# Optimization experiments

Hardware: AMD Instinct MI355X
Metric: run time of the kernel (lower is better)

## Reference

```python
import jax, jax.numpy as jnp
import numpy as np

N, E, G = 100000, 500000, 1000


def _gat(h_in, src, dst, W, a_s, a_d, b, n):
    # PyG GATConv, heads=1, concat=True, negative_slope=0.2, self-loops already in src/dst
    h = h_in @ W.T                                  # [N, out]
    alpha_src = h @ a_s                             # [N]
    alpha_dst = h @ a_d                             # [N]
    e = jax.nn.leaky_relu(alpha_src[src] + alpha_dst[dst], 0.2)  # [E']
    m = jax.ops.segment_max(e, dst, num_segments=n)
    ex = jnp.exp(e - m[dst])
    den = jax.ops.segment_sum(ex, dst, num_segments=n)
    alpha = ex / den[dst]                           # segment softmax over incoming edges
    out = jax.ops.segment_sum(h[src] * alpha[:, None], dst, num_segments=n)
    return out + b


def _forward(x, edge_index, batch, w1, b1, w2, b2, w3, b3,
             g1w, g1as, g1ad, g1b, g2w, g2as, g2ad, g2b,
             g3w, g3as, g3ad, g3b, g4w, g4as, g4ad, g4b,
             g5w, g5as, g5ad, g5b, lw, lb):
    n = x.shape[0]
    h = jax.nn.relu(x @ w1.T + b1)
    h = jax.nn.relu(h @ w2.T + b2)
    h = jax.nn.relu(h @ w3.T + b3)
    loops = jnp.arange(n)
    src = jnp.concatenate([edge_index[0], loops])   # add self-loops
    dst = jnp.concatenate([edge_index[1], loops])
    h = jax.nn.relu(_gat(h, src, dst, g1w, g1as, g1ad, g1b, n))
    h = jax.nn.relu(_gat(h, src, dst, g2w, g2as, g2ad, g2b, n))
    h = jax.nn.relu(_gat(h, src, dst, g3w, g3as, g3ad, g3b, n))
    h = jax.nn.relu(_gat(h, src, dst, g4w, g4as, g4ad, g4b, n))
    h = jax.nn.relu(_gat(h, src, dst, g5w, g5as, g5ad, g5b, n))
    sums = jax.ops.segment_sum(h, batch, num_segments=G)            # [G,32]
    cnt = jax.ops.segment_sum(jnp.ones((n,), h.dtype), batch, num_segments=G)
    mean = sums / jnp.maximum(cnt, 1.0)[:, None]
    return jax.nn.sigmoid(mean @ lw.T + lb)         # [G,1]


def setup_inputs() -> dict:
    key = jax.random.key(0)
    ks = jax.random.split(key, 24)

    def lin(k, o, i):
        k1, k2 = jax.random.split(k)
        s = 1.0 / np.sqrt(i)
        return (jax.random.uniform(k1, (o, i), jnp.float32, -s, s),
                jax.random.uniform(k2, (o,), jnp.float32, -s, s))

    def gat_p(k, i, o):
        k1, k2, k3 = jax.random.split(k, 3)
        s = 1.0 / np.sqrt(i)
        W = jax.random.uniform(k1, (o, i), jnp.float32, -s, s)
        a_s = jax.random.normal(k2, (o,), jnp.float32) / np.sqrt(o)
        a_d = jax.random.normal(k3, (o,), jnp.float32) / np.sqrt(o)
        return W, a_s, a_d, jnp.zeros((o,), jnp.float32)

    inp = {}
    inp['x'] = jax.random.normal(ks[0], (N, 1), jnp.float32)
    inp['edge_index'] = jax.random.randint(ks[1], (2, E), 0, N)
    inp['batch'] = jnp.sort(jax.random.randint(ks[2], (N,), 0, G))
    inp['w1'], inp['b1'] = lin(ks[3], 16, 1)
    inp['w2'], inp['b2'] = lin(ks[4], 32, 16)
    inp['w3'], inp['b3'] = lin(ks[5], 64, 32)
    dims = [(64, 128), (128, 256), (256, 128), (128, 64), (64, 32)]
    for j, (i, o) in enumerate(dims, start=1):
        W, a_s, a_d, b = gat_p(ks[5 + j], i, o)
        inp[f'g{j}w'], inp[f'g{j}as'], inp[f'g{j}ad'], inp[f'g{j}b'] = W, a_s, a_d, b
    inp['lw'], inp['lb'] = lin(ks[12], 1, 32)
    return inp


def reference(x, edge_index, batch, w1, b1, w2, b2, w3, b3,
              g1w, g1as, g1ad, g1b, g2w, g2as, g2ad, g2b,
              g3w, g3as, g3ad, g3b, g4w, g4as, g4ad, g4b,
              g5w, g5as, g5ad, g5b, lw, lb):
    return _forward(x, edge_index, batch, w1, b1, w2, b2, w3, b3,
                    g1w, g1as, g1ad, g1b, g2w, g2as, g2ad, g2b,
                    g3w, g3as, g3ad, g3b, g4w, g4as, g4ad, g4b,
                    g5w, g5as, g5ad, g5b, lw, lb)
```

## Files before the change

### kernel.cpp

```cpp
#include <hip/hip_runtime.h>
#include <math.h>

typedef __attribute__((ext_vector_type(8))) __bf16 bf16x8;
typedef __attribute__((ext_vector_type(4))) float f32x4;

__device__ inline unsigned short f2bf(float f) {
    unsigned int i = __float_as_uint(f);
    unsigned int r = i + 0x7fffu + ((i >> 16) & 1u);
    return (unsigned short)(r >> 16);
}
__device__ inline float bf2f(unsigned short u) {
    return __uint_as_float(((unsigned int)u) << 16);
}

__global__ __launch_bounds__(256) void prelude_kernel(
    const float* __restrict__ x,
    const float* __restrict__ w1, const float* __restrict__ b1,
    const float* __restrict__ w2, const float* __restrict__ b2,
    const float* __restrict__ w3, const float* __restrict__ b3,
    unsigned short* __restrict__ h0, int n,
    const float* __restrict__ g0, const float* __restrict__ g1, const float* __restrict__ g2,
    const float* __restrict__ g3, const float* __restrict__ g4,
    unsigned short* __restrict__ wbAll,
    const int* __restrict__ batch, int* __restrict__ gstart, int G,
    const int* __restrict__ dst, int* __restrict__ deg, int E,
    int mlpB, int f2bfB, int gsB, int histB,
    const float* __restrict__ as1, const float* __restrict__ ad1,
    float* __restrict__ s1out, float* __restrict__ d1out,
    const float* __restrict__ as2, const float* __restrict__ ad2,
    float* __restrict__ pv2) {
    int b = blockIdx.x;
    int tid = threadIdx.x;
    if (b < mlpB) {
        __shared__ float sw1[16], sb1[16], sw2[32 * 16], sb2[32], sw3[64 * 32], sb3[64];
        __shared__ float ps1[64], pd1[64];
        if (tid < 16) { sw1[tid] = w1[tid]; sb1[tid] = b1[tid]; }
        if (tid < 32) sb2[tid] = b2[tid];
        if (tid < 64) sb3[tid] = b3[tid];
        for (int i = tid; i < 512; i += 256) sw2[i] = w2[i];
        for (int i = tid; i < 2048; i += 256) sw3[i] = w3[i];
        if (tid >= 192) {
            int i = tid - 192;
            float s = 0.f, d = 0.f;
            for (int o = 0; o < 128; o++) {
                float w = g0[o * 64 + i];
                s += as1[o] * w;
                d += ad1[o] * w;
            }
            ps1[i] = s;
            pd1[i] = d;
        }
        __syncthreads();
        int node = b * 256 + tid;
        if (node >= n) return;
        float xv = x[node];
        float t1[16], t2[32];
#pragma unroll
        for (int i = 0; i < 16; i++) t1[i] = fmaxf(sw1[i] * xv + sb1[i], 0.f);
#pragma unroll
        for (int o = 0; o < 32; o++) {
            float a = sb2[o];
#pragma unroll
            for (int i = 0; i < 16; i++) a += sw2[o * 16 + i] * t1[i];
            t2[o] = fmaxf(a, 0.f);
        }
        float sdot = 0.f, ddot = 0.f;
        uint4* gp = (uint4*)(h0 + (size_t)node * 64);
#pragma unroll
        for (int c = 0; c < 8; c++) {
            unsigned int wvec[4];
#pragma unroll
            for (int p = 0; p < 4; p++) {
                int o = c * 8 + p * 2;
                float a0 = sb3[o], a1 = sb3[o + 1];
#pragma unroll
                for (int i = 0; i < 32; i++) {
                    a0 += sw3[o * 32 + i] * t2[i];
                    a1 += sw3[(o + 1) * 32 + i] * t2[i];
                }
                float r0 = fmaxf(a0, 0.f), r1 = fmaxf(a1, 0.f);
                sdot += r0 * ps1[o] + r1 * ps1[o + 1];
                ddot += r0 * pd1[o] + r1 * pd1[o + 1];
                wvec[p] = (unsigned)f2bf(r0) | ((unsigned)f2bf(r1) << 16);
            }
            gp[c] = make_uint4(wvec[0], wvec[1], wvec[2], wvec[3]);
        }
        s1out[node] = sdot;
        d1out[node] = ddot;
    } else if (b < mlpB + f2bfB) {
        int i = (b - mlpB) * 256 + tid;
        float v;
        if (i < 8192) v = g0[i];
        else if (i < 40960) v = g1[i - 8192];
        else if (i < 73728) v = g2[i - 40960];
        else if (i < 81920) v = g3[i - 73728];
        else if (i < 83968) v = g4[i - 81920];
        else return;
        wbAll[i] = f2bf(v);
    } else if (b < mlpB + f2bfB + gsB) {
        int g = (b - mlpB - f2bfB) * 256 + tid;
        if (g > G) return;
        if (g == G) { gstart[G] = n; return; }
        int lo = 0, hi = n;
        while (lo < hi) {
            int mid = (lo + hi) >> 1;
            if (batch[mid] < g) lo = mid + 1;
            else hi = mid;
        }
        gstart[g] = lo;
    } else if (b < mlpB + f2bfB + gsB + histB) {
        int e = (b - mlpB - f2bfB - gsB) * 256 + tid;
        if (e >= E + n) return;
        int d = (e < E) ? dst[e] : (e - E);
        atomicAdd(&deg[d], 1);
    } else {
        if (tid < 128) {
            float s = 0.f;
            for (int o = 0; o < 256; o++) s += as2[o] * g1[o * 128 + tid];
            pv2[tid] = s;
        } else {
            int c = tid - 128;
            float s = 0.f;
            for (int o = 0; o < 256; o++) s += ad2[o] * g1[o * 128 + c];
            pv2[128 + c] = s;
        }
    }
}

template <int BN, int EPI>
__global__ __launch_bounds__(256) void gemm_mfma(
    const unsigned short* __restrict__ A, const unsigned short* __restrict__ Wb,
    unsigned short* __restrict__ Cb,
    const float* __restrict__ avs, const float* __restrict__ avd,
    float* __restrict__ as_, float* __restrict__ ad_,
    const float* __restrict__ bias, int n, int K, int O) {
    constexpr int SN = BN / 32;
    __shared__ unsigned short As[128][72];
    __shared__ unsigned short Ws[BN][72];
    int tid = threadIdx.x;
    int row0 = blockIdx.x * 128, col0 = blockIdx.y * BN;
    int w = tid >> 6, lane = tid & 63;
    int wr = w >> 1, wc = w & 1;
    int quad = lane >> 4, l15 = lane & 15;
    f32x4 acc[4][SN];
#pragma unroll
    for (int mi = 0; mi < 4; mi++)
#pragma unroll
        for (int ni = 0; ni < SN; ni++) acc[mi][ni] = (f32x4){0.f, 0.f, 0.f, 0.f};

    for (int k0 = 0; k0 < K; k0 += 64) {
#pragma unroll
        for (int i = tid; i < 1024; i += 256) {
            int r = i >> 3, c8 = i & 7;
            int gr = row0 + r;
            uint4 v = make_uint4(0u, 0u, 0u, 0u);
            if (gr < n) v = *(const uint4*)(A + (size_t)gr * K + k0 + c8 * 8);
            *(uint4*)&As[r][c8 * 8] = v;
        }
#pragma unroll
        for (int i = tid; i < BN * 8; i += 256) {
            int r = i >> 3, c8 = i & 7;
            uint4 v = *(const uint4*)(Wb + (size_t)(col0 + r) * K + k0 + c8 * 8);
            *(uint4*)&Ws[r][c8 * 8] = v;
        }
        __syncthreads();
#pragma unroll
        for (int kk = 0; kk < 64; kk += 32) {
            bf16x8 bfr[SN];
#pragma unroll
            for (int ni = 0; ni < SN; ni++)
                bfr[ni] = *(const bf16x8*)&Ws[wc * (BN / 2) + ni * 16 + l15][kk + quad * 8];
#pragma unroll
            for (int mi = 0; mi < 4; mi++) {
                bf16x8 afr = *(const bf16x8*)&As[wr * 64 + mi * 16 + l15][kk + quad * 8];
#pragma unroll
                for (int ni = 0; ni < SN; ni++)
                    acc[mi][ni] = __builtin_amdgcn_mfma_f32_16x16x32_bf16(afr, bfr[ni],
                                                                          acc[mi][ni], 0, 0, 0);
            }
        }
        __syncthreads();
    }
    float avsv[SN], avdv[SN], bv[SN];
    int gc[SN];
#pragma unroll
    for (int ni = 0; ni < SN; ni++) {
        gc[ni] = col0 + wc * (BN / 2) + ni * 16 + l15;
        if constexpr (EPI != 2) {
            avsv[ni] = avs[gc[ni]];
            avdv[ni] = avd[gc[ni]];
        }
        if constexpr (EPI >= 1) bv[ni] = bias[gc[ni]];
    }
#pragma unroll
    for (int mi = 0; mi < 4; mi++) {
        int gm0 = row0 + wr * 64 + mi * 16 + quad * 4;
        float ps[4] = {0.f, 0.f, 0.f, 0.f}, pd[4] = {0.f, 0.f, 0.f, 0.f};
#pragma unroll
        for (int ni = 0; ni < SN; ni++) {
#pragma unroll
            for (int r = 0; r < 4; r++) {
                float d = acc[mi][ni][r];
                if constexpr (EPI >= 1) d = fmaxf(d + bv[ni], 0.f);
                int gm = gm0 + r;
                if (gm < n) Cb[(size_t)gm * O + gc[ni]] = f2bf(d);
                if constexpr (EPI != 2) {
                    ps[r] += d * avsv[ni];
                    pd[r] += d * avdv[ni];
                }
            }
        }
        if constexpr (EPI != 2) {
#pragma unroll
            for (int r = 0; r < 4; r++) {
#pragma unroll
                for (int m = 1; m <= 8; m <<= 1) {
                    ps[r] += __shfl_xor(ps[r], m);
                    pd[r] += __shfl_xor(pd[r], m);
                }
            }
            if (l15 == 0) {
#pragma unroll
                for (int r = 0; r < 4; r++) {
                    int gm = gm0 + r;
                    if (gm < n) {
                        atomicAdd(&as_[gm], ps[r]);
                        atomicAdd(&ad_[gm], pd[r]);
                    }
                }
            }
        }
    }
}

__global__ void scan_block_sums(const int* __restrict__ deg, int* __restrict__ bsums, int n) {
    __shared__ int sdata[256];
    int tid = threadIdx.x;
    int base = blockIdx.x * 1024 + tid * 4;
    int s = 0;
    for (int i = 0; i < 4; i++) {
        int g = base + i;
        if (g < n) s += deg[g];
    }
    sdata[tid] = s;
    __syncthreads();
    for (int off = 128; off > 0; off >>= 1) {
        if (tid < off) sdata[tid] += sdata[tid + off];
        __syncthreads();
    }
    if (tid == 0) bsums[blockIdx.x] = sdata[0];
}

__global__ void scan_write(const int* __restrict__ deg, const int* __restrict__ bsums,
                           int* __restrict__ rowptr, int* __restrict__ cursor, int n, int nb) {
    __shared__ int sdata[256];
    int tid = threadIdx.x;
    sdata[tid] = (tid < blockIdx.x && tid < nb) ? bsums[tid] : 0;
    __syncthreads();
    for (int off = 128; off > 0; off >>= 1) {
        if (tid < off) sdata[tid] += sdata[tid + off];
        __syncthreads();
    }
    int base = sdata[0];
    __syncthreads();
    int gbase = blockIdx.x * 1024 + tid * 4;
    int v[4];
    int s = 0;
    for (int i = 0; i < 4; i++) {
        int g = gbase + i;
        v[i] = (g < n) ? deg[g] : 0;
        s += v[i];
    }
    sdata[tid] = s;
    __syncthreads();
    for (int off = 1; off < 256; off <<= 1) {
        int t = (tid >= off) ? sdata[tid - off] : 0;
        __syncthreads();
        sdata[tid] += t;
        __syncthreads();
    }
    int excl = sdata[tid] - s + base;
    for (int i = 0; i < 4; i++) {
        int g = gbase + i;
        if (g < n) { rowptr[g] = excl; cursor[g] = excl; }
        excl += v[i];
    }
    if (blockIdx.x == gridDim.x - 1 && tid == 255) rowptr[n] = base + sdata[255];
}

__global__ void scatter_kernel(const int* __restrict__ esrc_in, const int* __restrict__ edst_in,
                               int* __restrict__ cursor, int* __restrict__ esrc, int E, int n) {
    int e = blockIdx.x * 256 + threadIdx.x;
    if (e >= E + n) return;
    int s, d;
    if (e < E) { s = esrc_in[e]; d = edst_in[e]; }
    else { s = e - E; d = e - E; }
    int pos = atomicAdd(&cursor[d], 1);
    esrc[pos] = s;
}

template <int O, bool BIASRELU>
__global__ __launch_bounds__(256) void gat_aggregate(
    const unsigned short* __restrict__ hl, const float* __restrict__ as_,
    const float* __restrict__ ad_, const int* __restrict__ rowptr,
    const int* __restrict__ esrc, const float* __restrict__ bias,
    unsigned short* __restrict__ hout, int n, float* __restrict__ zeroBuf, int zeroCnt) {
    int gtid = blockIdx.x * 256 + threadIdx.x;
    if (gtid < zeroCnt) zeroBuf[gtid] = 0.f;
    constexpr int C8 = O / 8;
    constexpr int EPP = 16 / C8;
    int tid = threadIdx.x;
    int v = blockIdx.x * 16 + (tid >> 4);
    int l = tid & 15;
    int gbase = tid & 48;
    if (v >= n) return;
    int beg = rowptr[v], end = rowptr[v + 1];
    int deg = end - beg;
    float adv = ad_[v];
    int sub = l / C8;
    int c = l % C8;
    float acc[8] = {0.f, 0.f, 0.f, 0.f, 0.f, 0.f, 0.f, 0.f};
    if (deg <= 16) {
        int sreg = v;
        float e = -1e30f;
        if (l < deg) {
            sreg = esrc[beg + l];
            float t = as_[sreg] + adv;
            e = (t > 0.f) ? t : 0.2f * t;
        }
        float m = e;
#pragma unroll
        for (int o = 8; o > 0; o >>= 1) m = fmaxf(m, __shfl_xor(m, o));
        float ex = (l < deg) ? __expf(e - m) : 0.f;
        float sum = ex;
#pragma unroll
        for (int o = 8; o > 0; o >>= 1) sum += __shfl_xor(sum, o);
        float alpha_r = ex / sum;
        for (int j0 = 0; j0 < deg; j0 += EPP) {
            int idx = j0 + sub;
            int cidx = (idx < deg) ? idx : 0;
            float alpha = __shfl(alpha_r, gbase + cidx);
            int s2 = __shfl(sreg, gbase + cidx);
            if (idx >= deg) alpha = 0.f;
            uint4 raw = ((const uint4*)(hl + (size_t)s2 * O))[c];
            acc[0] += alpha * __uint_as_float(raw.x << 16);
            acc[1] += alpha * __uint_as_float(raw.x & 0xffff0000u);
            acc[2] += alpha * __uint_as_float(raw.y << 16);
            acc[3] += alpha * __uint_as_float(raw.y & 0xffff0000u);
            acc[4] += alpha * __uint_as_float(raw.z << 16);
            acc[5] += alpha * __uint_as_float(raw.z & 0xffff0000u);
            acc[6] += alpha * __uint_as_float(raw.w << 16);
            acc[7] += alpha * __uint_as_float(raw.w & 0xffff0000u);
        }
    } else {
        float mymax = -1e30f;
        for (int j = beg + l; j < end; j += 16) {
            float e = as_[esrc[j]] + adv;
            e = (e > 0.f) ? e : 0.2f * e;
            mymax = fmaxf(mymax, e);
        }
#pragma unroll
        for (int o = 8; o > 0; o >>= 1) mymax = fmaxf(mymax, __shfl_xor(mymax, o));
        float mysum = 0.f;
        for (int j = beg + l; j < end; j += 16) {
            float e = as_[esrc[j]] + adv;
            e = (e > 0.f) ? e : 0.2f * e;
            mysum += __expf(e - mymax);
        }
#pragma unroll
        for (int o = 8; o > 0; o >>= 1) mysum += __shfl_xor(mysum, o);
        float invden = 1.f / mysum;
        for (int j0 = beg; j0 < end; j0 += EPP) {
            int j = j0 + sub;
            bool valid = j < end;
            int s = valid ? esrc[j] : v;
            float e = as_[s] + adv;
            e = (e > 0.f) ? e : 0.2f * e;
            float alpha = valid ? __expf(e - mymax) * invden : 0.f;
            uint4 raw = ((const uint4*)(hl + (size_t)s * O))[c];
            acc[0] += alpha * __uint_as_float(raw.x << 16);
            acc[1] += alpha * __uint_as_float(raw.x & 0xffff0000u);
            acc[2] += alpha * __uint_as_float(raw.y << 16);
            acc[3] += alpha * __uint_as_float(raw.y & 0xffff0000u);
            acc[4] += alpha * __uint_as_float(raw.z << 16);
            acc[5] += alpha * __uint_as_float(raw.z & 0xffff0000u);
            acc[6] += alpha * __uint_as_float(raw.w << 16);
            acc[7] += alpha * __uint_as_float(raw.w & 0xffff0000u);
        }
    }
#pragma unroll
    for (int o = C8; o < 16; o <<= 1)
#pragma unroll
        for (int k = 0; k < 8; k++) acc[k] += __shfl_xor(acc[k], o);
    if (l < C8) {
        unsigned short ov[8];
#pragma unroll
        for (int k = 0; k < 8; k++) {
            float val = acc[k];
            if constexpr (BIASRELU) val = fmaxf(val + bias[c * 8 + k], 0.f);
            ov[k] = f2bf(val);
        }
        uint4 packed;
        packed.x = (unsigned)ov[0] | ((unsigned)ov[1] << 16);
        packed.y = (unsigned)ov[2] | ((unsigned)ov[3] << 16);
        packed.z = (unsigned)ov[4] | ((unsigned)ov[5] << 16);
        packed.w = (unsigned)ov[6] | ((unsigned)ov[7] << 16);
        ((uint4*)(hout + (size_t)v * O))[c] = packed;
    }
}

__global__ __launch_bounds__(256) void pool_final_kernel(
    const unsigned short* __restrict__ h, const int* __restrict__ start,
    const float* __restrict__ lw, const float* __restrict__ lb,
    float* __restrict__ out, int G) {
    __shared__ float red[8][33];
    int g = blockIdx.x;
    if (g >= G) return;
    int beg = start[g], end = start[g + 1];
    int tid = threadIdx.x;
    int nodeLane = tid >> 5, f = tid & 31;
    float acc = 0.f;
    for (int v = beg + nodeLane; v < end; v += 8)
        acc += bf2f(h[(size_t)v * 32 + f]);
    red[nodeLane][f] = acc;
    __syncthreads();
    if (tid < 32) {
        float s = 0.f;
#pragma unroll
        for (int i = 0; i < 8; i++) s += red[i][f];
        float inv = 1.f / fmaxf((float)(end - beg), 1.f);
        float val = s * inv * lw[f];
#pragma unroll
        for (int o = 16; o > 0; o >>= 1) val += __shfl_xor(val, o);
        if (f == 0) out[g] = 1.f / (1.f + __expf(-(val + lb[0])));
    }
}

extern "C" void kernel_launch(void* const* d_in, const int* in_sizes, int n_in,
                              void* d_out, int out_size, void* d_ws, size_t ws_size,
                              hipStream_t stream) {
    const float* x = (const float*)d_in[0];
    const int* ei = (const int*)d_in[1];
    const int* batch = (const int*)d_in[2];
    const float* w1 = (const float*)d_in[3];
    const float* b1 = (const float*)d_in[4];
    const float* w2 = (const float*)d_in[5];
    const float* b2 = (const float*)d_in[6];
    const float* w3 = (const float*)d_in[7];
    const float* b3 = (const float*)d_in[8];
    const float* gw[5];
    const float* gas[5];
    const float* gad[5];
    const float* gb[5];
    for (int l = 0; l < 5; l++) {
        gw[l] = (const float*)d_in[9 + l * 4 + 0];
        gas[l] = (const float*)d_in[9 + l * 4 + 1];
        gad[l] = (const float*)d_in[9 + l * 4 + 2];
        gb[l] = (const float*)d_in[9 + l * 4 + 3];
    }
    const float* lw = (const float*)d_in[29];
    const float* lb = (const float*)d_in[30];
    float* out = (float*)d_out;

    int N = in_sizes[0];
    int E = in_sizes[1] / 2;
    int G = out_size;
    int Etot = E + N;

    char* ws = (char*)d_ws;
    size_t off = 0;
    auto alloc = [&](size_t bytes) -> void* {
        void* p = ws + off;
        off = (off + bytes + 255) & ~(size_t)255;
        return p;
    };
    unsigned short* actA = (unsigned short*)alloc((size_t)N * 256 * 2);
    unsigned short* actB = (unsigned short*)alloc((size_t)N * 256 * 2);
    char* zblock = (char*)alloc((size_t)N * 20);
    float* sd2 = (float*)zblock;
    float* sd3 = sd2 + (size_t)N * 2;
    int* deg = (int*)(zblock + (size_t)N * 16);
    float* sd1 = (float*)alloc((size_t)N * 2 * 4);
    float* pv2 = (float*)alloc(256 * 4);
    int* rowptr = (int*)alloc((size_t)(N + 1) * 4);
    int* cursor = (int*)alloc((size_t)(N + 1) * 4);
    int* esrc = (int*)alloc((size_t)Etot * 4);
    int* bsums = (int*)alloc(4096);
    int* gstart = (int*)alloc((size_t)(G + 1) * 4);
    unsigned short* wbAll = (unsigned short*)alloc((size_t)83968 * 2);
    const int woff[5] = {0, 8192, 40960, 73728, 81920};
    unsigned short* wb[5];
    for (int l = 0; l < 5; l++) wb[l] = wbAll + woff[l];
    (void)ws_size;
    (void)n_in;

    hipMemsetAsync(zblock, 0, (size_t)N * 20, stream);

    int mlpB = (N + 255) / 256;
    int f2bfB = (83968 + 255) / 256;
    int gsB = (G + 1 + 255) / 256;
    int histB = (Etot + 255) / 256;
    prelude_kernel<<<mlpB + f2bfB + gsB + histB + 1, 256, 0, stream>>>(
        x, w1, b1, w2, b2, w3, b3, actA, N, gw[0], gw[1], gw[2], gw[3], gw[4], wbAll, batch,
        gstart, G, ei + E, deg, E, mlpB, f2bfB, gsB, histB,
        gas[0], gad[0], sd1, sd1 + N, gas[1], gad[1], pv2);

    int nb = (N + 1023) / 1024;
    scan_block_sums<<<nb, 256, 0, stream>>>(deg, bsums, N);
    scan_write<<<nb, 256, 0, stream>>>(deg, bsums, rowptr, cursor, N, nb);
    scatter_kernel<<<(Etot + 255) / 256, 256, 0, stream>>>(ei, ei + E, cursor, esrc, E, N);

    int aggBlocks = (N + 15) / 16;
    int gx = (N + 127) / 128;

    gat_aggregate<64, false><<<aggBlocks, 256, 0, stream>>>(
        actA, sd1, sd1 + N, rowptr, esrc, nullptr, actB, N, nullptr, 0);
    {
        dim3 grid(gx, 2);
        gemm_mfma<64, 1><<<grid, 256, 0, stream>>>(actB, wb[0], actA, pv2, pv2 + 128, sd2,
                                                   sd2 + N, gb[0], N, 64, 128);
    }

    gat_aggregate<128, false><<<aggBlocks, 256, 0, stream>>>(
        actA, sd2, sd2 + N, rowptr, esrc, nullptr, actB, N, sd1, 2 * N);
    {
        dim3 grid(gx, 4);
        gemm_mfma<64, 2><<<grid, 256, 0, stream>>>(actB, wb[1], actA, nullptr, nullptr,
                                                   nullptr, nullptr, gb[1], N, 128, 256);
    }

    {
        dim3 grid(gx, 2);
        gemm_mfma<64, 0><<<grid, 256, 0, stream>>>(actA, wb[2], actB, gas[2], gad[2], sd3,
                                                   sd3 + N, nullptr, N, 256, 128);
    }
    gat_aggregate<128, true><<<aggBlocks, 256, 0, stream>>>(
        actB, sd3, sd3 + N, rowptr, esrc, gb[2], actA, N, sd2, 2 * N);

    {
        dim3 grid(gx, 1);
        gemm_mfma<64, 0><<<grid, 256, 0, stream>>>(actA, wb[3], actB, gas[3], gad[3], sd1,
                                                   sd1 + N, nullptr, N, 128, 64);
    }
    gat_aggregate<64, true><<<aggBlocks, 256, 0, stream>>>(
        actB, sd1, sd1 + N, rowptr, esrc, gb[3], actA, N, nullptr, 0);

    {
        dim3 grid(gx, 1);
        gemm_mfma<32, 0><<<grid, 256, 0, stream>>>(actA, wb[4], actB, gas[4], gad[4], sd2,
                                                   sd2 + N, nullptr, N, 64, 32);
    }
    gat_aggregate<32, true><<<aggBlocks, 256, 0, stream>>>(
        actB, sd2, sd2 + N, rowptr, esrc, gb[4], actA, N, nullptr, 0);

    pool_final_kernel<<<G, 256, 0, stream>>>(actA, gstart, lw, lb, out, G);
}
```

Baseline: 462.1 us.

## Read MLP weights directly from global memory and widen GEMM column tiles to 128

The prelude MLP no longer stages its weights in shared memory. It reads w1/w2/w3 straight from global memory as float4 vectors, which are uniform across threads and likely go to scalar or cached loads. The attention projection vectors are packed into one float4 shared array. Three GEMM launches now use 128-wide column tiles with half as many column blocks, so each block reuses its A tile across more outputs, at the cost of more registers per block and fewer blocks.

```diff
diff --git a/kernel.cpp b/kernel.cpp
--- a/kernel.cpp
+++ b/kernel.cpp
@@ -32,13 +32,7 @@
     int b = blockIdx.x;
     int tid = threadIdx.x;
     if (b < mlpB) {
-        __shared__ float sw1[16], sb1[16], sw2[32 * 16], sb2[32], sw3[64 * 32], sb3[64];
-        __shared__ float ps1[64], pd1[64];
-        if (tid < 16) { sw1[tid] = w1[tid]; sb1[tid] = b1[tid]; }
-        if (tid < 32) sb2[tid] = b2[tid];
-        if (tid < 64) sb3[tid] = b3[tid];
-        for (int i = tid; i < 512; i += 256) sw2[i] = w2[i];
-        for (int i = tid; i < 2048; i += 256) sw3[i] = w3[i];
+        __shared__ float4 psd1q[32];
         if (tid >= 192) {
             int i = tid - 192;
             float s = 0.f, d = 0.f;
@@ -47,8 +41,7 @@
                 s += as1[o] * w;
                 d += ad1[o] * w;
             }
-            ps1[i] = s;
-            pd1[i] = d;
+            ((float2*)psd1q)[i] = make_float2(s, d);
         }
         __syncthreads();
         int node = b * 256 + tid;
@@ -56,14 +49,20 @@
         float xv = x[node];
         float t1[16], t2[32];
 #pragma unroll
-        for (int i = 0; i < 16; i++) t1[i] = fmaxf(sw1[i] * xv + sb1[i], 0.f);
+        for (int i = 0; i < 16; i++) t1[i] = fmaxf(w1[i] * xv + b1[i], 0.f);
+        const float4* w2v = (const float4*)w2;
 #pragma unroll
         for (int o = 0; o < 32; o++) {
-            float a = sb2[o];
-#pragma unroll
-            for (int i = 0; i < 16; i++) a += sw2[o * 16 + i] * t1[i];
+            float a = b2[o];
+#pragma unroll
+            for (int q = 0; q < 4; q++) {
+                float4 wv = w2v[o * 4 + q];
+                a += wv.x * t1[q * 4] + wv.y * t1[q * 4 + 1] + wv.z * t1[q * 4 + 2] +
+                     wv.w * t1[q * 4 + 3];
+            }
             t2[o] = fmaxf(a, 0.f);
         }
+        const float4* w3v = (const float4*)w3;
         float sdot = 0.f, ddot = 0.f;
         uint4* gp = (uint4*)(h0 + (size_t)node * 64);
 #pragma unroll
@@ -72,15 +71,20 @@
 #pragma unroll
             for (int p = 0; p < 4; p++) {
                 int o = c * 8 + p * 2;
-                float a0 = sb3[o], a1 = sb3[o + 1];
-#pragma unroll
-                for (int i = 0; i < 32; i++) {
-                    a0 += sw3[o * 32 + i] * t2[i];
-                    a1 += sw3[(o + 1) * 32 + i] * t2[i];
+                float a0 = b3[o], a1 = b3[o + 1];
+#pragma unroll
+                for (int q = 0; q < 8; q++) {
+                    float4 wa = w3v[o * 8 + q];
+                    float4 wb = w3v[o * 8 + 8 + q];
+                    a0 += wa.x * t2[q * 4] + wa.y * t2[q * 4 + 1] + wa.z * t2[q * 4 + 2] +
+                          wa.w * t2[q * 4 + 3];
+                    a1 += wb.x * t2[q * 4] + wb.y * t2[q * 4 + 1] + wb.z * t2[q * 4 + 2] +
+                          wb.w * t2[q * 4 + 3];
                 }
                 float r0 = fmaxf(a0, 0.f), r1 = fmaxf(a1, 0.f);
-                sdot += r0 * ps1[o] + r1 * ps1[o + 1];
-                ddot += r0 * pd1[o] + r1 * pd1[o + 1];
+                float4 qsd = psd1q[o >> 1];
+                sdot += r0 * qsd.x + r1 * qsd.z;
+                ddot += r0 * qsd.y + r1 * qsd.w;
                 wvec[p] = (unsigned)f2bf(r0) | ((unsigned)f2bf(r1) << 16);
             }
             gp[c] = make_uint4(wvec[0], wvec[1], wvec[2], wvec[3]);
@@ -516,23 +520,23 @@
     gat_aggregate<64, false><<<aggBlocks, 256, 0, stream>>>(
         actA, sd1, sd1 + N, rowptr, esrc, nullptr, actB, N, nullptr, 0);
     {
-        dim3 grid(gx, 2);
-        gemm_mfma<64, 1><<<grid, 256, 0, stream>>>(actB, wb[0], actA, pv2, pv2 + 128, sd2,
-                                                   sd2 + N, gb[0], N, 64, 128);
+        dim3 grid(gx, 1);
+        gemm_mfma<128, 1><<<grid, 256, 0, stream>>>(actB, wb[0], actA, pv2, pv2 + 128, sd2,
+                                                    sd2 + N, gb[0], N, 64, 128);
     }
 
     gat_aggregate<128, false><<<aggBlocks, 256, 0, stream>>>(
         actA, sd2, sd2 + N, rowptr, esrc, nullptr, actB, N, sd1, 2 * N);
     {
-        dim3 grid(gx, 4);
-        gemm_mfma<64, 2><<<grid, 256, 0, stream>>>(actB, wb[1], actA, nullptr, nullptr,
-                                                   nullptr, nullptr, gb[1], N, 128, 256);
+        dim3 grid(gx, 2);
+        gemm_mfma<128, 2><<<grid, 256, 0, stream>>>(actB, wb[1], actA, nullptr, nullptr,
+                                                    nullptr, nullptr, gb[1], N, 128, 256);
     }
 
     {
-        dim3 grid(gx, 2);
-        gemm_mfma<64, 0><<<grid, 256, 0, stream>>>(actA, wb[2], actB, gas[2], gad[2], sd3,
-                                                   sd3 + N, nullptr, N, 256, 128);
+        dim3 grid(gx, 1);
+        gemm_mfma<128, 0><<<grid, 256, 0, stream>>>(actA, wb[2], actB, gas[2], gad[2], sd3,
+                                                    sd3 + N, nullptr, N, 256, 128);
     }
     gat_aggregate<128, true><<<aggBlocks, 256, 0, stream>>>(
         actB, sd3, sd3 + N, rowptr, esrc, gb[2], actA, N, sd2, 2 * N);
```

Measured after the change: 482.8 us. +4.5%, slower.
